# Performance work log

Measured on AMD Instinct MI355X. Metric: run time of the kernel, lower is better.

The kernel has to match this reference:

```python
import jax, jax.numpy as jnp
import numpy as np
from jax import lax

PAD = 1  # 3x3 conv, stride 1, padding 1


def conv2d(x, w, b=None):
    # x: [B,C,H,W], w: [O,I,3,3]
    y = lax.conv_general_dilated(x, w, window_strides=(1, 1),
                                 padding=((PAD, PAD), (PAD, PAD)),
                                 dimension_numbers=("NCHW", "OIHW", "NCHW"))
    if b is not None:
        y = y + b[None, :, None, None]
    return y


def _bilinear(img, py, px):
    # img: [C,H,W]; py,px: [K,H,W] sampling coords (float). Zero padding outside.
    H, W = img.shape[1], img.shape[2]
    y0 = jnp.floor(py)
    x0 = jnp.floor(px)
    wy = py - y0  # [K,H,W]
    wx = px - x0
    y0i = y0.astype(jnp.int32)
    x0i = x0.astype(jnp.int32)

    def gather(yi, xi):
        valid = ((yi >= 0) & (yi < H) & (xi >= 0) & (xi < W)).astype(img.dtype)
        yc = jnp.clip(yi, 0, H - 1)
        xc = jnp.clip(xi, 0, W - 1)
        return img[:, yc, xc] * valid[None]  # [C,K,H,W]

    v00 = gather(y0i, x0i)
    v01 = gather(y0i, x0i + 1)
    v10 = gather(y0i + 1, x0i)
    v11 = gather(y0i + 1, x0i + 1)
    return (v00 * (1 - wy) * (1 - wx) + v01 * (1 - wy) * wx
            + v10 * wy * (1 - wx) + v11 * wy * wx)  # [C,K,H,W]


def reference(x, w_offset, b_offset, w_mask, b_mask, w_conv):
    B, C, H, W = x.shape
    K = 9  # 3x3 kernel taps
    offset = conv2d(x, w_offset, b_offset)              # [B,2K,H,W]
    mask = jax.nn.sigmoid(conv2d(x, w_mask, b_mask))    # [B,K,H,W]

    off = offset.reshape(B, K, 2, H, W)
    dy = off[:, :, 0]  # [B,K,H,W] (torchvision layout: y first)
    dx = off[:, :, 1]

    k = jnp.arange(K)
    ky = (k // 3).astype(x.dtype) - PAD  # tap row offset in {-1,0,1}
    kx = (k % 3).astype(x.dtype) - PAD
    ii = jnp.arange(H, dtype=x.dtype)
    jj = jnp.arange(W, dtype=x.dtype)

    py = ii[None, None, :, None] + ky[None, :, None, None] + dy  # [B,K,H,W]
    px = jj[None, None, None, :] + kx[None, :, None, None] + dx

    sampled = jax.vmap(_bilinear)(x, py, px)  # [B,C,K,H,W]
    sampled = sampled * mask[:, None]          # modulated deform-conv v2

    # weight [64,3,3,3] -> [O,C,K]; contract over C and kernel taps
    out = jnp.einsum('bckhw,ock->bohw', sampled, w_conv.reshape(w_conv.shape[0], C, K))
    return out


def setup_inputs() -> dict:
    key = jax.random.key(0)
    k = jax.random.split(key, 6)
    B, C, H, W = 16, 3, 256, 256
    return {
        'x': jax.random.normal(k[0], (B, C, H, W), jnp.float32),
        'w_offset': jax.random.normal(k[1], (18, 3, 3, 3), jnp.float32) * 0.1,
        'b_offset': jax.random.normal(k[2], (18,), jnp.float32) * 0.1,
        'w_mask': jax.random.normal(k[3], (9, 3, 3, 3), jnp.float32) * 0.1,
        'b_mask': jax.random.normal(k[4], (9,), jnp.float32) * 0.1,
        'w_conv': jax.random.normal(k[5], (64, 3, 3, 3), jnp.float32) * 0.1,
    }
```

## Files before the change

### kernel.cpp

```cpp
#include <hip/hip_runtime.h>

#define HH 256
#define WW 256
#define CC 3
#define KK 9
#define OC 64
#define KD 27
#define PSTS 40
#define MOFF 5120
#define MST 16
#define WRB 6144
#define XST (4 * WRB)
#define XSLOT 1024

typedef __attribute__((ext_vector_type(8))) short bf16x8;
typedef __attribute__((ext_vector_type(4))) short s16x4;
typedef __attribute__((ext_vector_type(4))) float f32x4;
typedef __attribute__((ext_vector_type(2))) float f32x2;
typedef __attribute__((ext_vector_type(2))) unsigned int u32x2;

static __device__ __forceinline__ short f2bf(float f) {
    unsigned u = __float_as_uint(f);
    return (short)((u + 0x7fffu + ((u >> 16) & 1u)) >> 16);
}
static __device__ __forceinline__ unsigned pack2(short a, short b) {
    return (unsigned)(unsigned short)a | ((unsigned)(unsigned short)b << 16);
}
static __device__ __forceinline__ float bf2f(unsigned w) {
    return __uint_as_float(w << 16);
}
static __device__ __forceinline__ float bfup(unsigned w) {
    return __uint_as_float(w & 0xffff0000u);
}

__global__ __launch_bounds__(64) void dcn_prep(
    const float* __restrict__ w_offset, const float* __restrict__ b_offset,
    const float* __restrict__ w_mask,   const float* __restrict__ b_mask,
    const float* __restrict__ w_conv,
    short* __restrict__ wcf, char* __restrict__ wof)
{
    const int tid = threadIdx.x;
    const int fm = tid & 15, kc = tid >> 4;
#pragma unroll
    for (int t = 0; t < 4; ++t) {
        bf16x8 v;
#pragma unroll
        for (int e = 0; e < 8; ++e) {
            int kd = kc * 8 + e;
            v[e] = (kd < KD) ? f2bf(w_conv[(t * 16 + fm) * KD + kd]) : (short)0;
        }
        *(bf16x8*)(wcf + tid * 32 + t * 8) = v;
    }
#pragma unroll
    for (int t = 0; t < 2; ++t) {
        int ch = t * 16 + fm;
        bf16x8 vh, vl;
#pragma unroll
        for (int e = 0; e < 8; ++e) {
            int kd = kc * 8 + e;
            float val = 0.0f;
            if (kd < KD) {
                if (ch < 18) val = w_offset[ch * KD + kd];
                else if (ch < KD) val = w_mask[(ch - 18) * KD + kd];
            }
            unsigned u = __float_as_uint(val);
            vh[e] = (short)(u >> 16);
            float d = val - __uint_as_float(u & 0xffff0000u);
            vl[e] = (short)(__float_as_uint(d) >> 16);
        }
        *(bf16x8*)(wof + tid * 96 + t * 16) = vh;
        *(bf16x8*)(wof + tid * 96 + 32 + t * 16) = vl;
    }
#pragma unroll
    for (int t = 0; t < 2; ++t) {
        f32x4 cb;
#pragma unroll
        for (int r = 0; r < 4; ++r) {
            int ch = t * 16 + kc * 4 + r;
            float v = 0.0f;
            if (ch < 18) v = b_offset[ch];
            else if (ch < KD) v = b_mask[ch - 18];
            cb[r] = v;
        }
        *(f32x4*)(wof + tid * 96 + 64 + t * 16) = cb;
    }
}

__global__ __launch_bounds__(256) void dcn_main(
    const float* __restrict__ x,
    const short* __restrict__ wcf,
    const char*  __restrict__ wof,
    float* __restrict__ out)
{
    __shared__ __align__(16) char LDSBUF[XST + 7 * XSLOT * 2];

    const int tid = threadIdx.x;
    const int j = tid;
    const int i = blockIdx.x & (HH - 1);
    const int b = blockIdx.x >> 8;
    const int lane = tid & 63;
    const int wv = tid >> 6;
    const int fm = lane & 15;
    const int kc = lane >> 4;

    char* wbase = LDSBUF + wv * WRB;
    short* patchS = (short*)wbase;
    short* xs = (short*)(LDSBUF + XST);

    const float* xb = x + (size_t)b * (CC * HH * WW);

#pragma unroll
    for (int s = 0; s < 7; ++s) {
        int gr = min(max(i - 3 + s, 0), HH - 1);
        const float* rp = xb + (size_t)gr * WW + tid;
        float c0 = rp[0];
        float c1 = rp[HH * WW];
        float c2 = rp[2 * HH * WW];
        s16x4 v = {f2bf(c0), f2bf(c1), f2bf(c2), 0};
        *(s16x4*)(xs + s * XSLOT + tid * 4) = v;
    }
    __syncthreads();

    const bool yok0 = (i - 1) >= 0, yok2 = (i + 1) < HH;
    const bool xok0 = (j - 1) >= 0, xok2 = (j + 1) < WW;
    s16x4 pr[3][3];
#pragma unroll
    for (int p = 0; p < 3; ++p) {
#pragma unroll
        for (int q = 0; q < 3; ++q) {
            int xx = min(max(j + q - 1, 0), WW - 1);
            pr[p][q] = *(const s16x4*)(xs + (p + 2) * XSLOT + xx * 4);
        }
    }
    {
        short* rp = patchS + lane * PSTS;
#pragma unroll
        for (int o = 0; o < 4; ++o) {
            bf16x8 vh;
#pragma unroll
            for (int e = 0; e < 8; ++e) {
                int kd = o * 8 + e;
                if (kd < KD) {
                    int c = kd / 9, rem = kd - c * 9, p = rem / 3, q = rem - p * 3;
                    bool ok = (p == 0 ? yok0 : (p == 2 ? yok2 : true)) &&
                              (q == 0 ? xok0 : (q == 2 ? xok2 : true));
                    vh[e] = ok ? pr[p][q][c] : (short)0;
                } else {
                    vh[e] = (short)0;
                }
            }
            *(bf16x8*)(rp + o * 8) = vh;
        }
    }

    const char* wl = wof + lane * 96;
    bf16x8 whi0 = *(const bf16x8*)(wl);
    bf16x8 whi1 = *(const bf16x8*)(wl + 16);
    bf16x8 wlo0 = *(const bf16x8*)(wl + 32);
    bf16x8 wlo1 = *(const bf16x8*)(wl + 48);
    f32x4 cb0 = *(const f32x4*)(wl + 64);
    f32x4 cb1 = *(const f32x4*)(wl + 80);

    f32x4 dacc[4][2];
#pragma unroll
    for (int g = 0; g < 4; ++g) {
        bf16x8 phi = *(const bf16x8*)(patchS + (g * 16 + fm) * PSTS + kc * 8);
        f32x4 a0 = __builtin_amdgcn_mfma_f32_16x16x32_bf16(whi0, phi, cb0, 0, 0, 0);
        a0 = __builtin_amdgcn_mfma_f32_16x16x32_bf16(wlo0, phi, a0, 0, 0, 0);
        f32x4 a1 = __builtin_amdgcn_mfma_f32_16x16x32_bf16(whi1, phi, cb1, 0, 0, 0);
        a1 = __builtin_amdgcn_mfma_f32_16x16x32_bf16(wlo1, phi, a1, 0, 0, 0);
        dacc[g][0] = a0;
        dacc[g][1] = a1;
    }
#pragma unroll
    for (int g = 0; g < 4; ++g) {
        int r = g * 16 + fm;
        char* dr = wbase + r * 80;
        char* mr = wbase + MOFF + r * MST;
        *(f32x4*)(dr + kc * 16) = dacc[g][0];
        f32x4 a1 = dacc[g][1];
        if (kc == 0) {
            *(f32x2*)(dr + 64) = (f32x2){a1[0], a1[1]};
            *(unsigned*)(dr + 72) = pack2(f2bf(a1[2]), f2bf(a1[3]));
        } else if (kc == 1) {
            *(unsigned*)(dr + 76) = pack2(f2bf(a1[0]), f2bf(a1[1]));
            *(unsigned*)(mr + 0) = pack2(f2bf(a1[2]), f2bf(a1[3]));
        } else if (kc == 2) {
            *(unsigned*)(mr + 4) = pack2(f2bf(a1[0]), f2bf(a1[1]));
            *(unsigned short*)(mr + 8) = (unsigned short)f2bf(a1[2]);
        }
    }

    const char* myD = wbase + lane * 80;
    f32x4 d03 = *(const f32x4*)(myD);
    f32x4 d47 = *(const f32x4*)(myD + 16);
    f32x4 d8b = *(const f32x4*)(myD + 32);
    f32x4 dcf = *(const f32x4*)(myD + 48);
    f32x2 d8p = *(const f32x2*)(myD + 64);
    u32x2 z03 = *(const u32x2*)(myD + 72);
    const char* myM = wbase + MOFF + lane * MST;
    u32x2 z47 = *(const u32x2*)(myM);
    unsigned z8w = *(const unsigned short*)(myM + 8);

    const float dyv[9] = {d03[0], d03[2], d47[0], d47[2], d8b[0], d8b[2], dcf[0], dcf[2], d8p[0]};
    const float dxv[9] = {d03[1], d03[3], d47[1], d47[3], d8b[1], d8b[3], dcf[1], dcf[3], d8p[1]};
    const float mzf[9] = {bf2f(z03.x), bfup(z03.x), bf2f(z03.y), bfup(z03.y),
                          bf2f(z47.x), bfup(z47.x), bf2f(z47.y), bfup(z47.y), bf2f(z8w)};

    bf16x8 afrag[4];
#pragma unroll
    for (int t2 = 0; t2 < 4; ++t2) afrag[t2] = *(const bf16x8*)(wcf + lane * 32 + t2 * 8);

    const float* x0p = xb;
    const float* x1p = xb + (size_t)HH * WW;
    const float* x2p = xb + (size_t)2 * HH * WW;
    float s27[KD];
#pragma unroll
    for (int k = 0; k < KK; ++k) {
        float dy = dyv[k], dx = dxv[k];
        float msk = 1.0f / (1.0f + __expf(-mzf[k]));

        float py = (float)(i + (k / 3) - 1) + dy;
        float px = (float)(j + (k % 3) - 1) + dx;
        float y0f = floorf(py), x0f = floorf(px);
        float wy = py - y0f, wx = px - x0f;
        int y0 = (int)y0f, x0 = (int)x0f;
        int y1 = y0 + 1, x1 = x0 + 1;

        float w00 = (1.0f - wy) * (1.0f - wx);
        float w01 = (1.0f - wy) * wx;
        float w10 = wy * (1.0f - wx);
        float w11 = wy * wx;

        bool v0y = (unsigned)y0 < HH, v1y = (unsigned)y1 < HH;
        bool v0x = (unsigned)x0 < WW, v1x = (unsigned)x1 < WW;
        float f00 = (v0y && v0x) ? w00 : 0.0f;
        float f01 = (v0y && v1x) ? w01 : 0.0f;
        float f10 = (v1y && v0x) ? w10 : 0.0f;
        float f11 = (v1y && v1x) ? w11 : 0.0f;

        int y0c = min(max(y0, 0), HH - 1), y1c = min(max(y1, 0), HH - 1);
        int s0 = y0c - i + 3;
        int s1 = y1c - i + 3;
        float r0, r1, r2;
        if (__builtin_expect(__any(((unsigned)s0 > 6u) || ((unsigned)s1 > 6u)), 0)) {
            int x0c = min(max(x0, 0), WW - 1), x1c = min(max(x1, 0), WW - 1);
            int o00 = y0c * WW + x0c, o01 = y0c * WW + x1c;
            int o10 = y1c * WW + x0c, o11 = y1c * WW + x1c;
            r0 = x0p[o00] * f00 + x0p[o01] * f01 + x0p[o10] * f10 + x0p[o11] * f11;
            r1 = x1p[o00] * f00 + x1p[o01] * f01 + x1p[o10] * f10 + x1p[o11] * f11;
            r2 = x2p[o00] * f00 + x2p[o01] * f01 + x2p[o10] * f10 + x2p[o11] * f11;
        } else {
            int xl = min(max(x0, 0), WW - 2);
            bool sw = (x0 != xl);
            const short* p0 = xs + s0 * XSLOT + xl * 4;
            const short* p1 = xs + s1 * XSLOT + xl * 4;
            u32x2 lo0 = *(const u32x2*)p0;
            u32x2 hi0 = *(const u32x2*)(p0 + 4);
            u32x2 lo1 = *(const u32x2*)p1;
            u32x2 hi1 = *(const u32x2*)(p1 + 4);

            float a0 = sw ? f01 : f00, b0 = sw ? f00 : f01;
            float a1w = sw ? f11 : f10, b1w = sw ? f10 : f11;

            r0 = fmaf(bf2f(lo0.x), a0, fmaf(bf2f(hi0.x), b0,
                 fmaf(bf2f(lo1.x), a1w, bf2f(hi1.x) * b1w)));
            r1 = fmaf(bfup(lo0.x), a0, fmaf(bfup(hi0.x), b0,
                 fmaf(bfup(lo1.x), a1w, bfup(hi1.x) * b1w)));
            r2 = fmaf(bf2f(lo0.y), a0, fmaf(bf2f(hi0.y), b0,
                 fmaf(bf2f(lo1.y), a1w, bf2f(hi1.y) * b1w)));
        }
        s27[k]      = r0 * msk;
        s27[9 + k]  = r1 * msk;
        s27[18 + k] = r2 * msk;
    }

    {
        short* srow = patchS + lane * PSTS;
#pragma unroll
        for (int o = 0; o < 4; ++o) {
            bf16x8 v;
#pragma unroll
            for (int e = 0; e < 8; ++e) {
                int kd = o * 8 + e;
                v[e] = (kd < KD) ? f2bf(s27[kd]) : (short)0;
            }
            *(bf16x8*)(srow + o * 8) = v;
        }
    }

    float* obase = out + ((size_t)b * OC * HH + i) * WW;
#pragma unroll
    for (int g = 0; g < 4; ++g) {
        bf16x8 sfrag = *(const bf16x8*)(patchS + (g * 16 + fm) * PSTS + kc * 8);
#pragma unroll
        for (int t2 = 0; t2 < 4; ++t2) {
            f32x4 acc = (f32x4){0.f, 0.f, 0.f, 0.f};
            acc = __builtin_amdgcn_mfma_f32_16x16x32_bf16(sfrag, afrag[t2], acc, 0, 0, 0);
            float* op = obase + (size_t)(t2 * 16 + fm) * (HH * WW) + (wv * 64 + g * 16 + kc * 4);
            *(f32x4*)op = acc;
        }
    }
}

extern "C" void kernel_launch(void* const* d_in, const int* in_sizes, int n_in,
                              void* d_out, int out_size, void* d_ws, size_t ws_size,
                              hipStream_t stream) {
    const float* x        = (const float*)d_in[0];
    const float* w_offset = (const float*)d_in[1];
    const float* b_offset = (const float*)d_in[2];
    const float* w_mask   = (const float*)d_in[3];
    const float* b_mask   = (const float*)d_in[4];
    const float* w_conv   = (const float*)d_in[5];
    float* out = (float*)d_out;

    int B = in_sizes[0] / (CC * HH * WW);

    short* wcf = (short*)d_ws;
    char*  wof = (char*)d_ws + 4096;

    hipLaunchKernelGGL(dcn_prep, dim3(1), dim3(64), 0, stream,
                       w_offset, b_offset, w_mask, b_mask, w_conv, wcf, wof);
    hipLaunchKernelGGL(dcn_main, dim3(B * HH), dim3(256), 0, stream,
                       x, wcf, wof, out);
}
```

Baseline: 78.66 us.

## Pre-convert input to packed channel-interleaved bf16 in prep kernel

The prep kernel now also converts the whole input tensor from planar fp32 to a pixel-interleaved bf16x4 layout in workspace. The main kernel then loads each of its seven halo rows with a single 8-byte load per thread, replacing three strided fp32 loads plus conversion. This removes the roughly 7x redundant fp32 reads and conversions across row blocks, at the cost of an extra full pass over the input and a workspace write and read. The bf16 rounding helper also switches to the library conversion intrinsic.

Result: faster. 75.84 us (-3.6%).

```diff
diff --git a/kernel.cpp b/kernel.cpp
--- a/kernel.cpp
+++ b/kernel.cpp
@@ -1,4 +1,5 @@
 #include <hip/hip_runtime.h>
+#include <hip/hip_bf16.h>
 
 #define HH 256
 #define WW 256
@@ -20,8 +21,8 @@
 typedef __attribute__((ext_vector_type(2))) unsigned int u32x2;
 
 static __device__ __forceinline__ short f2bf(float f) {
-    unsigned u = __float_as_uint(f);
-    return (short)((u + 0x7fffu + ((u >> 16) & 1u)) >> 16);
+    __hip_bfloat16 h = __float2bfloat16(f);
+    return __builtin_bit_cast(short, h);
 }
 static __device__ __forceinline__ unsigned pack2(short a, short b) {
     return (unsigned)(unsigned short)a | ((unsigned)(unsigned short)b << 16);
@@ -33,61 +34,86 @@
     return __uint_as_float(w & 0xffff0000u);
 }
 
-__global__ __launch_bounds__(64) void dcn_prep(
+__global__ __launch_bounds__(256) void dcn_prep(
+    const float* __restrict__ x,
     const float* __restrict__ w_offset, const float* __restrict__ b_offset,
     const float* __restrict__ w_mask,   const float* __restrict__ b_mask,
     const float* __restrict__ w_conv,
-    short* __restrict__ wcf, char* __restrict__ wof)
+    short* __restrict__ xbf, short* __restrict__ wcf, char* __restrict__ wof,
+    int npix)
 {
     const int tid = threadIdx.x;
-    const int fm = tid & 15, kc = tid >> 4;
-#pragma unroll
-    for (int t = 0; t < 4; ++t) {
-        bf16x8 v;
-#pragma unroll
-        for (int e = 0; e < 8; ++e) {
-            int kd = kc * 8 + e;
-            v[e] = (kd < KD) ? f2bf(w_conv[(t * 16 + fm) * KD + kd]) : (short)0;
-        }
-        *(bf16x8*)(wcf + tid * 32 + t * 8) = v;
-    }
-#pragma unroll
-    for (int t = 0; t < 2; ++t) {
-        int ch = t * 16 + fm;
-        bf16x8 vh, vl;
-#pragma unroll
-        for (int e = 0; e < 8; ++e) {
-            int kd = kc * 8 + e;
-            float val = 0.0f;
-            if (kd < KD) {
-                if (ch < 18) val = w_offset[ch * KD + kd];
-                else if (ch < KD) val = w_mask[(ch - 18) * KD + kd];
-            }
-            unsigned u = __float_as_uint(val);
-            vh[e] = (short)(u >> 16);
-            float d = val - __uint_as_float(u & 0xffff0000u);
-            vl[e] = (short)(__float_as_uint(d) >> 16);
-        }
-        *(bf16x8*)(wof + tid * 96 + t * 16) = vh;
-        *(bf16x8*)(wof + tid * 96 + 32 + t * 16) = vl;
-    }
-#pragma unroll
-    for (int t = 0; t < 2; ++t) {
-        f32x4 cb;
-#pragma unroll
-        for (int r = 0; r < 4; ++r) {
-            int ch = t * 16 + kc * 4 + r;
-            float v = 0.0f;
-            if (ch < 18) v = b_offset[ch];
-            else if (ch < KD) v = b_mask[ch - 18];
-            cb[r] = v;
-        }
-        *(f32x4*)(wof + tid * 96 + 64 + t * 16) = cb;
-    }
+    if (blockIdx.x == gridDim.x - 1) {
+        if (tid < 64) {
+            const int fm = tid & 15, kc = tid >> 4;
+#pragma unroll
+            for (int t = 0; t < 4; ++t) {
+                bf16x8 v;
+#pragma unroll
+                for (int e = 0; e < 8; ++e) {
+                    int kd = kc * 8 + e;
+                    v[e] = (kd < KD) ? f2bf(w_conv[(t * 16 + fm) * KD + kd]) : (short)0;
+                }
+                *(bf16x8*)(wcf + tid * 32 + t * 8) = v;
+            }
+#pragma unroll
+            for (int t = 0; t < 2; ++t) {
+                int ch = t * 16 + fm;
+                bf16x8 vh, vl;
+#pragma unroll
+                for (int e = 0; e < 8; ++e) {
+                    int kd = kc * 8 + e;
+                    float val = 0.0f;
+                    if (kd < KD) {
+                        if (ch < 18) val = w_offset[ch * KD + kd];
+                        else if (ch < KD) val = w_mask[(ch - 18) * KD + kd];
+                    }
+                    unsigned u = __float_as_uint(val);
+                    vh[e] = (short)(u >> 16);
+                    float d = val - __uint_as_float(u & 0xffff0000u);
+                    vl[e] = (short)(__float_as_uint(d) >> 16);
+                }
+                *(bf16x8*)(wof + tid * 96 + t * 16) = vh;
+                *(bf16x8*)(wof + tid * 96 + 32 + t * 16) = vl;
+            }
+#pragma unroll
+            for (int t = 0; t < 2; ++t) {
+                f32x4 cb;
+#pragma unroll
+                for (int r = 0; r < 4; ++r) {
+                    int ch = t * 16 + kc * 4 + r;
+                    float v = 0.0f;
+                    if (ch < 18) v = b_offset[ch];
+                    else if (ch < KD) v = b_mask[ch - 18];
+                    cb[r] = v;
+                }
+                *(f32x4*)(wof + tid * 96 + 64 + t * 16) = cb;
+            }
+        }
+        return;
+    }
+
+    const int p0 = (blockIdx.x * 256 + tid) * 4;
+    if (p0 >= npix) return;
+    const int bb = p0 >> 16;
+    const int q  = p0 & 0xffff;
+    const float* xb = x + (size_t)bb * (3 * 65536) + q;
+    f32x4 r0 = *(const f32x4*)(xb);
+    f32x4 r1 = *(const f32x4*)(xb + 65536);
+    f32x4 r2 = *(const f32x4*)(xb + 131072);
+
+    bf16x8 v0 = {f2bf(r0[0]), f2bf(r1[0]), f2bf(r2[0]), 0,
+                 f2bf(r0[1]), f2bf(r1[1]), f2bf(r2[1]), 0};
+    bf16x8 v1 = {f2bf(r0[2]), f2bf(r1[2]), f2bf(r2[2]), 0,
+                 f2bf(r0[3]), f2bf(r1[3]), f2bf(r2[3]), 0};
+    short* A = xbf + (size_t)p0 * 4;
+    *(bf16x8*)A       = v0;
+    *(bf16x8*)(A + 8) = v1;
 }
 
 __global__ __launch_bounds__(256) void dcn_main(
     const float* __restrict__ x,
+    const short* __restrict__ xbf,
     const short* __restrict__ wcf,
     const char*  __restrict__ wof,
     float* __restrict__ out)
@@ -108,16 +134,17 @@
     short* xs = (short*)(LDSBUF + XST);
 
     const float* xb = x + (size_t)b * (CC * HH * WW);
-
+    const short* xrow = xbf + (size_t)b * (HH * WW * 4);
+
+    u32x2 st[7];
 #pragma unroll
     for (int s = 0; s < 7; ++s) {
         int gr = min(max(i - 3 + s, 0), HH - 1);
-        const float* rp = xb + (size_t)gr * WW + tid;
-        float c0 = rp[0];
-        float c1 = rp[HH * WW];
-        float c2 = rp[2 * HH * WW];
-        s16x4 v = {f2bf(c0), f2bf(c1), f2bf(c2), 0};
-        *(s16x4*)(xs + s * XSLOT + tid * 4) = v;
+        st[s] = *(const u32x2*)(xrow + ((size_t)gr * WW + tid) * 4);
+    }
+#pragma unroll
+    for (int s = 0; s < 7; ++s) {
+        *(u32x2*)(xs + s * XSLOT + tid * 4) = st[s];
     }
     __syncthreads();
 
@@ -315,12 +342,16 @@
     float* out = (float*)d_out;
 
     int B = in_sizes[0] / (CC * HH * WW);
-
-    short* wcf = (short*)d_ws;
-    char*  wof = (char*)d_ws + 4096;
-
-    hipLaunchKernelGGL(dcn_prep, dim3(1), dim3(64), 0, stream,
-                       w_offset, b_offset, w_mask, b_mask, w_conv, wcf, wof);
+    int npix = B * HH * WW;
+
+    short* xbf = (short*)d_ws;
+    short* wcf = (short*)((char*)d_ws + (size_t)npix * 8);
+    char*  wof = (char*)d_ws + (size_t)npix * 8 + 4096;
+
+    int nb = (npix + 1023) / 1024;
+    hipLaunchKernelGGL(dcn_prep, dim3(nb + 1), dim3(256), 0, stream,
+                       x, w_offset, b_offset, w_mask, b_mask, w_conv,
+                       xbf, wcf, wof, npix);
     hipLaunchKernelGGL(dcn_main, dim3(B * HH), dim3(256), 0, stream,
-                       x, wcf, wof, out);
-}
+                       x, xbf, wcf, wof, out);
+}
```
